# Kernel tuning notes

Hardware: AMD Instinct MI355X
Metric: run time of the kernel (lower is better)

## Reference

```python
import jax, jax.numpy as jnp
import numpy as np

N_HEADS = 8
N_HIDDEN = 64  # out_features // n_heads
SLOPE = 0.2
NEG = -9e15


def setup_inputs() -> dict:
    key = jax.random.key(0)
    k1, k2, k3, k4, k5 = jax.random.split(key, 5)
    B, N, F_in, F_out = 4, 2048, 512, 512
    h = jax.random.normal(k1, (B, N, F_in), dtype=jnp.float32)
    adj = jax.random.randint(k2, (B, N, N), 0, 2, dtype=jnp.int32)
    # xavier_uniform with gain=1.414: limit = gain*sqrt(6/(fan_in+fan_out))
    lim_W = 1.414 * np.sqrt(6.0 / (F_in + F_out))
    W_l = jax.random.uniform(k3, (F_in, F_out), jnp.float32, -lim_W, lim_W)
    W_r = jax.random.uniform(k4, (F_in, F_out), jnp.float32, -lim_W, lim_W)
    lim_a = 1.414 * np.sqrt(6.0 / (N_HIDDEN + 1))
    a = jax.random.uniform(k5, (N_HIDDEN, 1), jnp.float32, -lim_a, lim_a)
    return {"h": h, "adj": adj, "W_l": W_l, "W_r": W_r, "a": a}


def reference(h, adj, W_l, W_r, a):
    B, N, _ = h.shape
    H, d = N_HEADS, N_HIDDEN
    # torch .view(-1, H, N, d) is a raw row-major reshape, replicated exactly here
    Wh_l = jax.nn.leaky_relu((h @ W_l).reshape(B, H, N, d), SLOPE)
    Wh_r = jax.nn.leaky_relu((h @ W_r).reshape(B, H, N, d), SLOPE)
    # e: [B,H,N,1] + [B,H,1,N] -> [B,H,N,N]
    e = Wh_l @ a + jnp.swapaxes(Wh_r @ a, 2, 3)
    att = jnp.where(adj[:, None, :, :] > 0, e, NEG)
    att = jax.nn.softmax(att, axis=-1)
    h_prime = att @ Wh_r  # [B,H,N,d]
    # torch .view(-1, N, H*d): raw reshape (no head transpose)
    out = jax.nn.elu(h_prime.reshape(B, N, H * d))
    return out
```

## Files before the change

kernel.cpp:

```cpp
#include <hip/hip_runtime.h>

#define NB   4
#define NN   2048
#define FIN  512
#define FOUT 512
#define NHD  8
#define DH   64
#define VC   576
#define SLOPE 0.2f

typedef __attribute__((ext_vector_type(8)))  short bhalf8;
typedef __attribute__((ext_vector_type(16))) float f32x16;

__device__ __forceinline__ void load_lds16(const void* g, void* l) {
  __builtin_amdgcn_global_load_lds(
      (const __attribute__((address_space(1))) unsigned int*)g,
      (__attribute__((address_space(3))) unsigned int*)l, 16, 0, 0);
}

__device__ __forceinline__ unsigned int bfpair(float lo, float hi) {
  unsigned int a = __float_as_uint(lo), b = __float_as_uint(hi);
  a = (a + 0x7FFFu + ((a >> 16) & 1u)) >> 16;
  b = (b + 0x7FFFu + ((b >> 16) & 1u)) & 0xFFFF0000u;
  return a | b;
}

__device__ __forceinline__ void split2(float x, float y,
                                       unsigned int& hp, unsigned int& lp) {
  unsigned int ux = __float_as_uint(x), uy = __float_as_uint(y);
  unsigned int rx = (ux + 0x7FFFu + ((ux >> 16) & 1u)) & 0xFFFF0000u;
  unsigned int ry = (uy + 0x7FFFu + ((uy >> 16) & 1u)) & 0xFFFF0000u;
  float lx = x - __uint_as_float(rx);
  float ly = y - __uint_as_float(ry);
  unsigned int vx = __float_as_uint(lx), vy = __float_as_uint(ly);
  hp = (rx >> 16) | ry;
  lp = ((vx + 0x7FFFu + ((vx >> 16) & 1u)) >> 16)
     | ((vy + 0x7FFFu + ((vy >> 16) & 1u)) & 0xFFFF0000u);
}

__global__ __launch_bounds__(256) void k_split_prep(
    const float* __restrict__ h,
    unsigned short* __restrict__ hHi, unsigned short* __restrict__ hLo,
    const float* __restrict__ Wr,
    unsigned short* __restrict__ wTh, unsigned short* __restrict__ wTl)
{
  __shared__ float s[64][65];
  const int t = threadIdx.x;
  if (blockIdx.x < 2048) {
    size_t base = ((size_t)blockIdx.x * 256 + t) * 8;
    float4 a = *(const float4*)(h + base);
    float4 b = *(const float4*)(h + base + 4);
    uint4 uh, ul;
    split2(a.x, a.y, uh.x, ul.x);
    split2(a.z, a.w, uh.y, ul.y);
    split2(b.x, b.y, uh.z, ul.z);
    split2(b.z, b.w, uh.w, ul.w);
    *(uint4*)(hHi + base) = uh;
    *(uint4*)(hLo + base) = ul;
    return;
  }
  const int bid2 = blockIdx.x - 2048;
  const int n0 = (bid2 & 7) * 64, k0 = (bid2 >> 3) * 64;
#pragma unroll
  for (int p = 0; p < 4; ++p) {
    int row = p * 16 + (t >> 4);
    int col = (t & 15) * 4;
    float4 v = *(const float4*)(Wr + (size_t)(k0 + row) * FOUT + n0 + col);
    s[row][col] = v.x; s[row][col+1] = v.y; s[row][col+2] = v.z; s[row][col+3] = v.w;
  }
  __syncthreads();
  const int n = t >> 2;
  const int ks = (t & 3) * 16;
  uint4 h0, h1, l0, l1;
  split2(s[ks+ 0][n], s[ks+ 1][n], h0.x, l0.x);
  split2(s[ks+ 2][n], s[ks+ 3][n], h0.y, l0.y);
  split2(s[ks+ 4][n], s[ks+ 5][n], h0.z, l0.z);
  split2(s[ks+ 6][n], s[ks+ 7][n], h0.w, l0.w);
  split2(s[ks+ 8][n], s[ks+ 9][n], h1.x, l1.x);
  split2(s[ks+10][n], s[ks+11][n], h1.y, l1.y);
  split2(s[ks+12][n], s[ks+13][n], h1.z, l1.z);
  split2(s[ks+14][n], s[ks+15][n], h1.w, l1.w);
  size_t o = (size_t)(n0 + n) * FIN + k0 + ks;
  *(uint4*)(wTh + o) = h0; *(uint4*)(wTh + o + 8) = h1;
  *(uint4*)(wTl + o) = l0; *(uint4*)(wTl + o + 8) = l1;
}

__global__ __launch_bounds__(256) void k_gemm_whr_mfma(
    const unsigned short* __restrict__ hHi, const unsigned short* __restrict__ hLo,
    const unsigned short* __restrict__ wTh, const unsigned short* __restrict__ wTl,
    float* __restrict__ Whr, const float* __restrict__ av, float* __restrict__ er)
{
  __shared__ unsigned short sAh[128*64], sAl[128*64];
  __shared__ unsigned short sBh[64*64],  sBl[64*64];
  const int tid = threadIdx.x, lane = tid & 63, wv = tid >> 6;
  const int Bid = blockIdx.x;
  const int g8 = Bid & 7, idx = Bid >> 3;
  const int sg = idx >> 3, ct = idx & 7;
  const int c0 = ct * 64;
  const int row0 = (g8 * 8 + sg) * 128;

  const unsigned short* pAh[4]; const unsigned short* pAl[4];
  unsigned short *dAh[4], *dAl[4];
#pragma unroll
  for (int t = 0; t < 4; ++t) {
    int I  = wv + t * 4;
    int rl = I * 8 + (lane >> 3);
    int gk = (lane & 7) ^ (rl & 7);
    pAh[t] = hHi + (size_t)(row0 + rl) * FIN + gk * 8;
    pAl[t] = hLo + (size_t)(row0 + rl) * FIN + gk * 8;
    dAh[t] = sAh + I * 512;  dAl[t] = sAl + I * 512;
  }
  const unsigned short* pBh[2]; const unsigned short* pBl[2];
  unsigned short *dBh[2], *dBl[2];
#pragma unroll
  for (int t = 0; t < 2; ++t) {
    int I  = wv + t * 4;
    int rl = I * 8 + (lane >> 3);
    int gk = (lane & 7) ^ (rl & 7);
    pBh[t] = wTh + (size_t)(c0 + rl) * FIN + gk * 8;
    pBl[t] = wTl + (size_t)(c0 + rl) * FIN + gk * 8;
    dBh[t] = sBh + I * 512;  dBl[t] = sBl + I * 512;
  }

  const int wi = wv >> 1, wc = wv & 1;
  const int l31 = lane & 31, half = lane >> 5;
  const int aoff0 = (wi*64 +      l31) * 64;
  const int aoff1 = (wi*64 + 32 + l31) * 64;
  const int boff  = (wc*32 +      l31) * 64;
  f32x16 acc0 = {}; f32x16 acc1 = {};

  for (int k0 = 0; k0 < FIN; k0 += 64) {
#pragma unroll
    for (int t = 0; t < 4; ++t) { load_lds16(pAh[t] + k0, dAh[t]);
                                  load_lds16(pAl[t] + k0, dAl[t]); }
#pragma unroll
    for (int t = 0; t < 2; ++t) { load_lds16(pBh[t] + k0, dBh[t]);
                                  load_lds16(pBl[t] + k0, dBl[t]); }
    __syncthreads();
#pragma unroll
    for (int kb = 0; kb < 4; ++kb) {
      int kg = ((kb*2 + half) ^ (lane & 7)) * 8;
      bhalf8 bh  = *(const bhalf8*)&sBh[boff  + kg];
      bhalf8 bl  = *(const bhalf8*)&sBl[boff  + kg];
      bhalf8 a0h = *(const bhalf8*)&sAh[aoff0 + kg];
      bhalf8 a0l = *(const bhalf8*)&sAl[aoff0 + kg];
      bhalf8 a1h = *(const bhalf8*)&sAh[aoff1 + kg];
      bhalf8 a1l = *(const bhalf8*)&sAl[aoff1 + kg];
      acc0 = __builtin_amdgcn_mfma_f32_32x32x16_bf16(a0h, bh, acc0, 0, 0, 0);
      acc1 = __builtin_amdgcn_mfma_f32_32x32x16_bf16(a1h, bh, acc1, 0, 0, 0);
      acc0 = __builtin_amdgcn_mfma_f32_32x32x16_bf16(a0l, bh, acc0, 0, 0, 0);
      acc1 = __builtin_amdgcn_mfma_f32_32x32x16_bf16(a1l, bh, acc1, 0, 0, 0);
      acc0 = __builtin_amdgcn_mfma_f32_32x32x16_bf16(a0h, bl, acc0, 0, 0, 0);
      acc1 = __builtin_amdgcn_mfma_f32_32x32x16_bf16(a1h, bl, acc1, 0, 0, 0);
    }
    __syncthreads();
  }

  const float a_d = av[wc*32 + l31];
#pragma unroll
  for (int mi = 0; mi < 2; ++mi) {
    const f32x16 a = mi ? acc1 : acc0;
#pragma unroll
    for (int reg = 0; reg < 16; ++reg) {
      int grow = row0 + wi*64 + mi*32 + ((reg & 3) + 8*(reg >> 2) + 4*half);
      int b  = grow >> 11;
      int n  = grow & 2047;
      int hd = n >> 8;
      int jj = ((n & 255) << 3) | ct;
      int dd = wc*32 + l31;
      float v = a[reg];
      v = v > 0.f ? v : SLOPE * v;
      Whr[(((size_t)(b*NHD + hd)) * NN + jj) * DH + dd] = v;
      float p = v * a_d;
      p += __shfl_xor(p, 16, 32);
      p += __shfl_xor(p,  8, 32);
      p += __shfl_xor(p,  4, 32);
      p += __shfl_xor(p,  2, 32);
      p += __shfl_xor(p,  1, 32);
      if (l31 == 0)
        unsafeAtomicAdd(er + ((size_t)(b*NHD + hd)) * NN + jj, p);
    }
  }
}

__global__ __launch_bounds__(256) void k_softmax_w(float* __restrict__ er)
{
  __shared__ float wm[4];
  float* p = er + (size_t)blockIdx.x * NN;
  float m = -1e30f;
  for (int j = threadIdx.x; j < NN; j += 256) m = fmaxf(m, p[j]);
#pragma unroll
  for (int off = 32; off; off >>= 1) m = fmaxf(m, __shfl_down(m, off, 64));
  if ((threadIdx.x & 63) == 0) wm[threadIdx.x >> 6] = m;
  __syncthreads();
  float mm = fmaxf(fmaxf(wm[0], wm[1]), fmaxf(wm[2], wm[3]));
  for (int j = threadIdx.x; j < NN; j += 256) p[j] = expf(p[j] - mm);
}

__global__ __launch_bounds__(256) void k_build_vt(
    const float* __restrict__ Whr, const float* __restrict__ w,
    unsigned short* __restrict__ Vt)
{
  const int lane = threadIdx.x & 63, wv = threadIdx.x >> 6;
  const int c = blockIdx.y * 4 + wv;
  const int b = blockIdx.z;
  const int j = blockIdx.x * 512 + lane * 8;
  uint4 o = {0u, 0u, 0u, 0u};
  if (c < 512) {
    const int hh = c >> 6, dd = c & 63;
    const size_t r = ((size_t)(b*NHD + hh))*NN + j;
    const float* wp = w + r;
    const float* hp = Whr + r*DH + dd;
    float v[8];
#pragma unroll
    for (int q = 0; q < 8; ++q) v[q] = wp[q] * hp[(size_t)q*DH];
    o.x = bfpair(v[0], v[1]); o.y = bfpair(v[2], v[3]);
    o.z = bfpair(v[4], v[5]); o.w = bfpair(v[6], v[7]);
  } else if (c < 520) {
    const size_t r = ((size_t)(b*NHD + (c - 512)))*NN + j;
    float4 a0 = *(const float4*)(w + r);
    float4 a1 = *(const float4*)(w + r + 4);
    o.x = bfpair(a0.x, a0.y); o.y = bfpair(a0.z, a0.w);
    o.z = bfpair(a1.x, a1.y); o.w = bfpair(a1.z, a1.w);
  }
  *(uint4*)(Vt + ((size_t)(b*VC + c))*NN + j) = o;
}

__global__ __launch_bounds__(256) void k_attn_mfma(
    const int* __restrict__ adj, const unsigned short* __restrict__ Vt,
    float* __restrict__ C)
{
  __shared__ unsigned short sA[128][72];
  __shared__ unsigned short sB[64][64];
  const int tid = threadIdx.x;
  const int lane = tid & 63, wv = tid >> 6;
  const int Bid = blockIdx.x;
  const int g8 = Bid & 7;
  const int kh = (Bid >> 3) & 1;
  const int idx = Bid >> 4;
  const int ct = idx >> 3, sg = idx & 7;
  const int c0 = ct * 64;
  const int row0 = (g8 * 8 + sg) * 128;
  const int b = row0 >> 11;

  const unsigned short* pB[2];
  unsigned short* dB[2];
#pragma unroll
  for (int t = 0; t < 2; ++t) {
    int I  = wv + t*4;
    int rl = I*8 + (lane >> 3);
    int gk = (lane & 7) ^ (rl & 7);
    pB[t] = Vt + ((size_t)(b*VC + c0 + rl))*NN + gk*8;
    dB[t] = &sB[0][0] + I*512;
  }
  const int* adjp = adj + (size_t)b*NN*NN + (size_t)(row0 & 2047)*NN
                    + (tid >> 3)*NN + (tid & 7)*8;
  unsigned short* sAp = &sA[tid >> 3][(tid & 7)*8];

  const int wi = wv >> 1, wc = wv & 1;
  const int l31 = lane & 31, half = lane >> 5;
  f32x16 acc0 = {}; f32x16 acc1 = {};
  const unsigned short* aRd0 = &sA[wi*64 +      l31][half*8];
  const unsigned short* aRd1 = &sA[wi*64 + 32 + l31][half*8];
  const int nloc = wc*32 + l31;

  const int kbeg = kh * 1024, kend = kbeg + 1024;
  for (int k0 = kbeg; k0 < kend; k0 += 64) {
    load_lds16(pB[0] + k0, dB[0]);
    load_lds16(pB[1] + k0, dB[1]);
#pragma unroll
    for (int rr = 0; rr < 4; ++rr) {
      const int* p = adjp + rr*32*NN + k0;
      int4 q0 = *(const int4*)p;
      int4 q1 = *(const int4*)(p + 4);
      uint4 u;
      u.x = (unsigned)(q0.x | (q0.y << 16)) * 0x3F80u;
      u.y = (unsigned)(q0.z | (q0.w << 16)) * 0x3F80u;
      u.z = (unsigned)(q1.x | (q1.y << 16)) * 0x3F80u;
      u.w = (unsigned)(q1.z | (q1.w << 16)) * 0x3F80u;
      *(uint4*)(sAp + rr*32*72) = u;
    }
    __syncthreads();
#pragma unroll
    for (int kb = 0; kb < 4; ++kb) {
      int kg = (kb*2 + half) ^ (lane & 7);
      bhalf8 bf = *(const bhalf8*)&sB[nloc][kg*8];
      bhalf8 a0 = *(const bhalf8*)(aRd0 + kb*16);
      bhalf8 a1 = *(const bhalf8*)(aRd1 + kb*16);
      acc0 = __builtin_amdgcn_mfma_f32_32x32x16_bf16(a0, bf, acc0, 0, 0, 0);
      acc1 = __builtin_amdgcn_mfma_f32_32x32x16_bf16(a1, bf, acc1, 0, 0, 0);
    }
    __syncthreads();
  }
  float* Cp = C + ((size_t)(row0 + wi*64))*VC + c0 + wc*32 + l31;
#pragma unroll
  for (int mi = 0; mi < 2; ++mi) {
    const f32x16 a = mi ? acc1 : acc0;
#pragma unroll
    for (int reg = 0; reg < 16; ++reg) {
      int irow = (reg & 3) + 8*(reg >> 2) + 4*half + mi*32;
      unsafeAtomicAdd(Cp + (size_t)irow * VC, a[reg]);
    }
  }
}

__global__ __launch_bounds__(256) void k_epilogue(
    const float* __restrict__ C, float* __restrict__ out)
{
  int idx = blockIdx.x * 256 + threadIdx.x;
  int d  = idx & 63;
  int t  = idx >> 6;
  int hh = t & 7;
  int bi = t >> 3;
  int i  = bi & 2047, b = bi >> 11;
  float num = C[(size_t)bi * VC + (hh << 6) + d];
  float den = C[(size_t)bi * VC + 512 + hh];
  float v = num / den;
  v = v > 0.f ? v : expm1f(v);
  int n = (hh << 8) | (i >> 3);
  int f = ((i & 7) << 6) | d;
  out[((size_t)b * NN + n) * FOUT + f] = v;
}

extern "C" void kernel_launch(void* const* d_in, const int* in_sizes, int n_in,
                              void* d_out, int out_size, void* d_ws, size_t ws_size,
                              hipStream_t stream)
{
  const float* hin = (const float*)d_in[0];
  const int*   adj = (const int*)d_in[1];
  const float* Wr  = (const float*)d_in[3];
  const float* av  = (const float*)d_in[4];
  float* out = (float*)d_out;

  char* ws = (char*)d_ws;
  unsigned short* hHi = (unsigned short*)(ws);
  unsigned short* hLo = (unsigned short*)(ws + 8388608);
  unsigned short* wTh = (unsigned short*)(ws + 16777216);
  unsigned short* wTl = (unsigned short*)(ws + 17301504);
  float* Whr  = (float*)(ws + 17825792);
  float* wexp = (float*)(ws + 34603008);
  unsigned short* Vt = (unsigned short*)(ws);
  float* C    = (float*)(ws + 17825792);

  hipMemsetAsync(wexp, 0, (size_t)NB*NHD*NN*4, stream);
  k_split_prep   <<<dim3(2112),           256, 0, stream>>>(hin, hHi, hLo, Wr, wTh, wTl);
  k_gemm_whr_mfma<<<dim3(512),            256, 0, stream>>>(hHi, hLo, wTh, wTl, Whr, av, wexp);
  k_softmax_w    <<<dim3(NB*NHD),         256, 0, stream>>>(wexp);
  k_build_vt     <<<dim3(NN/512, VC/4, NB), 256, 0, stream>>>(Whr, wexp, Vt);
  hipMemsetAsync(C, 0, (size_t)NB*NN*VC*4, stream);
  k_attn_mfma    <<<dim3(1152),           256, 0, stream>>>(adj, Vt, C);
  k_epilogue     <<<dim3(NB*NN*FOUT/256), 256, 0, stream>>>(C, out);
}
```

Measured before the change: 237.8 us.

## Fuse softmax weights, Vt build and epilogue into attention pipeline, drop atomics

The softmax-exponent and Vt-build kernels are merged into one kernel that transposes through shared memory to write coalesced bf16 Vt rows. The attention kernel no longer splits K across two blocks. It computes the denominator with an extra MFMA per K-step and applies the divide and ELU directly, removing the C buffer, both memsets, the atomic accumulation and the separate epilogue kernel. The GEMM's er reduction now goes through LDS with a plain store instead of atomics. The tradeoffs are half as many attention blocks (512 vs 1152), each doing a full-length K loop, and every softmax block recomputing the per-row max.

New measurement: 198.8 us. 1.2x faster.

```diff
diff --git a/kernel.cpp b/kernel.cpp
--- a/kernel.cpp
+++ b/kernel.cpp
@@ -6,7 +6,7 @@
 #define FOUT 512
 #define NHD  8
 #define DH   64
-#define VC   576
+#define VTR  520
 #define SLOPE 0.2f
 
 typedef __attribute__((ext_vector_type(8)))  short bhalf8;
@@ -18,11 +18,9 @@
       (__attribute__((address_space(3))) unsigned int*)l, 16, 0, 0);
 }
 
-__device__ __forceinline__ unsigned int bfpair(float lo, float hi) {
-  unsigned int a = __float_as_uint(lo), b = __float_as_uint(hi);
-  a = (a + 0x7FFFu + ((a >> 16) & 1u)) >> 16;
-  b = (b + 0x7FFFu + ((b >> 16) & 1u)) & 0xFFFF0000u;
-  return a | b;
+__device__ __forceinline__ unsigned short bfrne(float x) {
+  unsigned int u = __float_as_uint(x);
+  return (unsigned short)((u + 0x7FFFu + ((u >> 16) & 1u)) >> 16);
 }
 
 __device__ __forceinline__ void split2(float x, float y,
@@ -92,6 +90,7 @@
 {
   __shared__ unsigned short sAh[128*64], sAl[128*64];
   __shared__ unsigned short sBh[64*64],  sBl[64*64];
+  __shared__ float erT[128][2];
   const int tid = threadIdx.x, lane = tid & 63, wv = tid >> 6;
   const int Bid = blockIdx.x;
   const int g8 = Bid & 7, idx = Bid >> 3;
@@ -162,112 +161,130 @@
     const f32x16 a = mi ? acc1 : acc0;
 #pragma unroll
     for (int reg = 0; reg < 16; ++reg) {
-      int grow = row0 + wi*64 + mi*32 + ((reg & 3) + 8*(reg >> 2) + 4*half);
+      int rmap = (reg & 3) + 8*(reg >> 2) + 4*half;
+      int rowloc = wi*64 + mi*32 + rmap;
+      int grow = row0 + rowloc;
       int b  = grow >> 11;
       int n  = grow & 2047;
       int hd = n >> 8;
       int jj = ((n & 255) << 3) | ct;
-      int dd = wc*32 + l31;
       float v = a[reg];
       v = v > 0.f ? v : SLOPE * v;
-      Whr[(((size_t)(b*NHD + hd)) * NN + jj) * DH + dd] = v;
+      Whr[(((size_t)(b*NHD + hd)) * NN + jj) * DH + (wc*32 + l31)] = v;
       float p = v * a_d;
       p += __shfl_xor(p, 16, 32);
       p += __shfl_xor(p,  8, 32);
       p += __shfl_xor(p,  4, 32);
       p += __shfl_xor(p,  2, 32);
       p += __shfl_xor(p,  1, 32);
-      if (l31 == 0)
-        unsafeAtomicAdd(er + ((size_t)(b*NHD + hd)) * NN + jj, p);
-    }
-  }
-}
-
-__global__ __launch_bounds__(256) void k_softmax_w(float* __restrict__ er)
+      if (l31 == 0) erT[rowloc][wc] = p;
+    }
+  }
+  __syncthreads();
+  if (tid < 128) {
+    int grow = row0 + tid;
+    int b  = grow >> 11;
+    int n  = grow & 2047;
+    int hd = n >> 8;
+    int jj = ((n & 255) << 3) | ct;
+    er[((size_t)(b*NHD + hd)) * NN + jj] = erT[tid][0] + erT[tid][1];
+  }
+}
+
+__global__ __launch_bounds__(256) void k_softvt(
+    const float* __restrict__ Whr, const float* __restrict__ er,
+    unsigned short* __restrict__ Vt)
 {
   __shared__ float wm[4];
-  float* p = er + (size_t)blockIdx.x * NN;
+  __shared__ float wbuf[256];
+  __shared__ unsigned short tile[64][264];
+  const int tid = threadIdx.x;
+  const int jc = blockIdx.x, hh = blockIdx.y, b = blockIdx.z;
+  const float* ep = er + ((size_t)(b*NHD + hh)) * NN;
   float m = -1e30f;
-  for (int j = threadIdx.x; j < NN; j += 256) m = fmaxf(m, p[j]);
+  for (int j = tid; j < NN; j += 256) m = fmaxf(m, ep[j]);
 #pragma unroll
   for (int off = 32; off; off >>= 1) m = fmaxf(m, __shfl_down(m, off, 64));
-  if ((threadIdx.x & 63) == 0) wm[threadIdx.x >> 6] = m;
-  __syncthreads();
-  float mm = fmaxf(fmaxf(wm[0], wm[1]), fmaxf(wm[2], wm[3]));
-  for (int j = threadIdx.x; j < NN; j += 256) p[j] = expf(p[j] - mm);
-}
-
-__global__ __launch_bounds__(256) void k_build_vt(
-    const float* __restrict__ Whr, const float* __restrict__ w,
-    unsigned short* __restrict__ Vt)
-{
-  const int lane = threadIdx.x & 63, wv = threadIdx.x >> 6;
-  const int c = blockIdx.y * 4 + wv;
-  const int b = blockIdx.z;
-  const int j = blockIdx.x * 512 + lane * 8;
-  uint4 o = {0u, 0u, 0u, 0u};
-  if (c < 512) {
-    const int hh = c >> 6, dd = c & 63;
-    const size_t r = ((size_t)(b*NHD + hh))*NN + j;
-    const float* wp = w + r;
-    const float* hp = Whr + r*DH + dd;
-    float v[8];
-#pragma unroll
-    for (int q = 0; q < 8; ++q) v[q] = wp[q] * hp[(size_t)q*DH];
-    o.x = bfpair(v[0], v[1]); o.y = bfpair(v[2], v[3]);
-    o.z = bfpair(v[4], v[5]); o.w = bfpair(v[6], v[7]);
-  } else if (c < 520) {
-    const size_t r = ((size_t)(b*NHD + (c - 512)))*NN + j;
-    float4 a0 = *(const float4*)(w + r);
-    float4 a1 = *(const float4*)(w + r + 4);
-    o.x = bfpair(a0.x, a0.y); o.y = bfpair(a0.z, a0.w);
-    o.z = bfpair(a1.x, a1.y); o.w = bfpair(a1.z, a1.w);
-  }
-  *(uint4*)(Vt + ((size_t)(b*VC + c))*NN + j) = o;
-}
-
-__global__ __launch_bounds__(256) void k_attn_mfma(
+  if ((tid & 63) == 0) wm[tid >> 6] = m;
+  __syncthreads();
+  const float mm = fmaxf(fmaxf(wm[0], wm[1]), fmaxf(wm[2], wm[3]));
+  const int j0 = jc * 256;
+  float w = expf(ep[j0 + tid] - mm);
+  wbuf[tid] = w;
+  Vt[((size_t)(b*VTR + 512 + hh)) * NN + j0 + tid] = bfrne(w);
+  __syncthreads();
+  const size_t wbase = ((size_t)(b*NHD + hh)) * NN;
+#pragma unroll
+  for (int p = 0; p < 16; ++p) {
+    int jr = p*16 + (tid >> 4);
+    int dc = (tid & 15) * 4;
+    float4 v = *(const float4*)(Whr + (wbase + j0 + jr) * DH + dc);
+    float wj = wbuf[jr];
+    tile[dc+0][jr] = bfrne(v.x * wj);
+    tile[dc+1][jr] = bfrne(v.y * wj);
+    tile[dc+2][jr] = bfrne(v.z * wj);
+    tile[dc+3][jr] = bfrne(v.w * wj);
+  }
+  __syncthreads();
+#pragma unroll
+  for (int q = 0; q < 8; ++q) {
+    int idx = q*256 + tid;
+    int d = idx >> 5, seg = idx & 31;
+    uint4 t16 = *(const uint4*)&tile[d][seg*8];
+    *(uint4*)(Vt + ((size_t)(b*VTR + hh*64 + d)) * NN + j0 + seg*8) = t16;
+  }
+}
+
+__global__ __launch_bounds__(256) void k_attn_out(
     const int* __restrict__ adj, const unsigned short* __restrict__ Vt,
-    float* __restrict__ C)
+    float* __restrict__ out)
 {
   __shared__ unsigned short sA[128][72];
-  __shared__ unsigned short sB[64][64];
+  __shared__ unsigned short sB[96][64];
+  __shared__ float denL[128];
   const int tid = threadIdx.x;
   const int lane = tid & 63, wv = tid >> 6;
   const int Bid = blockIdx.x;
-  const int g8 = Bid & 7;
-  const int kh = (Bid >> 3) & 1;
-  const int idx = Bid >> 4;
-  const int ct = idx >> 3, sg = idx & 7;
-  const int c0 = ct * 64;
-  const int row0 = (g8 * 8 + sg) * 128;
+  const int g8 = Bid & 7, rest = Bid >> 3;
+  const int ct = rest & 7, sg = rest >> 3;
+  const int row0 = (g8*8 + sg) * 128;
   const int b = row0 >> 11;
 
-  const unsigned short* pB[2];
-  unsigned short* dB[2];
+  const unsigned short* pB[3];
+  unsigned short* dB[3];
 #pragma unroll
   for (int t = 0; t < 2; ++t) {
     int I  = wv + t*4;
     int rl = I*8 + (lane >> 3);
     int gk = (lane & 7) ^ (rl & 7);
-    pB[t] = Vt + ((size_t)(b*VC + c0 + rl))*NN + gk*8;
+    pB[t] = Vt + ((size_t)(b*VTR + ct*64 + rl))*NN + gk*8;
     dB[t] = &sB[0][0] + I*512;
   }
+  {
+    int x  = lane >> 3;
+    int gk = (lane & 7) ^ (x & 7);
+    pB[2] = Vt + ((size_t)(b*VTR + 512 + x))*NN + gk*8;
+    dB[2] = &sB[0][0] + 8*512;
+  }
+  for (int idx = tid; idx < 384; idx += 256)
+    ((uint4*)&sB[72][0])[idx] = uint4{0u,0u,0u,0u};
+
   const int* adjp = adj + (size_t)b*NN*NN + (size_t)(row0 & 2047)*NN
                     + (tid >> 3)*NN + (tid & 7)*8;
   unsigned short* sAp = &sA[tid >> 3][(tid & 7)*8];
 
   const int wi = wv >> 1, wc = wv & 1;
   const int l31 = lane & 31, half = lane >> 5;
-  f32x16 acc0 = {}; f32x16 acc1 = {};
+  f32x16 acc0 = {}; f32x16 acc1 = {}; f32x16 acc2 = {};
   const unsigned short* aRd0 = &sA[wi*64 +      l31][half*8];
   const unsigned short* aRd1 = &sA[wi*64 + 32 + l31][half*8];
+  const unsigned short* aRd2 = &sA[wv*32 +      l31][half*8];
   const int nloc = wc*32 + l31;
 
-  const int kbeg = kh * 1024, kend = kbeg + 1024;
-  for (int k0 = kbeg; k0 < kend; k0 += 64) {
+  for (int k0 = 0; k0 < NN; k0 += 64) {
     load_lds16(pB[0] + k0, dB[0]);
     load_lds16(pB[1] + k0, dB[1]);
+    if (wv == 0) load_lds16(pB[2] + k0, dB[2]);
 #pragma unroll
     for (int rr = 0; rr < 4; ++rr) {
       const int* p = adjp + rr*32*NN + k0;
@@ -284,42 +301,38 @@
 #pragma unroll
     for (int kb = 0; kb < 4; ++kb) {
       int kg = (kb*2 + half) ^ (lane & 7);
-      bhalf8 bf = *(const bhalf8*)&sB[nloc][kg*8];
+      bhalf8 bf  = *(const bhalf8*)&sB[nloc][kg*8];
+      bhalf8 bf2 = *(const bhalf8*)&sB[64 + l31][kg*8];
       bhalf8 a0 = *(const bhalf8*)(aRd0 + kb*16);
       bhalf8 a1 = *(const bhalf8*)(aRd1 + kb*16);
-      acc0 = __builtin_amdgcn_mfma_f32_32x32x16_bf16(a0, bf, acc0, 0, 0, 0);
-      acc1 = __builtin_amdgcn_mfma_f32_32x32x16_bf16(a1, bf, acc1, 0, 0, 0);
+      bhalf8 a2 = *(const bhalf8*)(aRd2 + kb*16);
+      acc0 = __builtin_amdgcn_mfma_f32_32x32x16_bf16(a0, bf,  acc0, 0, 0, 0);
+      acc1 = __builtin_amdgcn_mfma_f32_32x32x16_bf16(a1, bf,  acc1, 0, 0, 0);
+      acc2 = __builtin_amdgcn_mfma_f32_32x32x16_bf16(a2, bf2, acc2, 0, 0, 0);
     }
     __syncthreads();
   }
-  float* Cp = C + ((size_t)(row0 + wi*64))*VC + c0 + wc*32 + l31;
+  if (l31 == ct) {
+#pragma unroll
+    for (int reg = 0; reg < 16; ++reg)
+      denL[wv*32 + (reg & 3) + 8*(reg >> 2) + 4*half] = acc2[reg];
+  }
+  __syncthreads();
+  const int ib = row0 & 2047;
 #pragma unroll
   for (int mi = 0; mi < 2; ++mi) {
     const f32x16 a = mi ? acc1 : acc0;
 #pragma unroll
     for (int reg = 0; reg < 16; ++reg) {
-      int irow = (reg & 3) + 8*(reg >> 2) + 4*half + mi*32;
-      unsafeAtomicAdd(Cp + (size_t)irow * VC, a[reg]);
-    }
-  }
-}
-
-__global__ __launch_bounds__(256) void k_epilogue(
-    const float* __restrict__ C, float* __restrict__ out)
-{
-  int idx = blockIdx.x * 256 + threadIdx.x;
-  int d  = idx & 63;
-  int t  = idx >> 6;
-  int hh = t & 7;
-  int bi = t >> 3;
-  int i  = bi & 2047, b = bi >> 11;
-  float num = C[(size_t)bi * VC + (hh << 6) + d];
-  float den = C[(size_t)bi * VC + 512 + hh];
-  float v = num / den;
-  v = v > 0.f ? v : expm1f(v);
-  int n = (hh << 8) | (i >> 3);
-  int f = ((i & 7) << 6) | d;
-  out[((size_t)b * NN + n) * FOUT + f] = v;
+      int il = wi*64 + mi*32 + (reg & 3) + 8*(reg >> 2) + 4*half;
+      int i  = ib + il;
+      float v = a[reg] / denL[il];
+      v = v > 0.f ? v : expm1f(v);
+      int n = (ct << 8) | (i >> 3);
+      int f = ((i & 7) << 6) | nloc;
+      out[((size_t)b*NN + n)*FOUT + f] = v;
+    }
+  }
 }
 
 extern "C" void kernel_launch(void* const* d_in, const int* in_sizes, int n_in,
@@ -338,16 +351,11 @@
   unsigned short* wTh = (unsigned short*)(ws + 16777216);
   unsigned short* wTl = (unsigned short*)(ws + 17301504);
   float* Whr  = (float*)(ws + 17825792);
-  float* wexp = (float*)(ws + 34603008);
+  float* er   = (float*)(ws + 34603008);
   unsigned short* Vt = (unsigned short*)(ws);
-  float* C    = (float*)(ws + 17825792);
-
-  hipMemsetAsync(wexp, 0, (size_t)NB*NHD*NN*4, stream);
-  k_split_prep   <<<dim3(2112),           256, 0, stream>>>(hin, hHi, hLo, Wr, wTh, wTl);
-  k_gemm_whr_mfma<<<dim3(512),            256, 0, stream>>>(hHi, hLo, wTh, wTl, Whr, av, wexp);
-  k_softmax_w    <<<dim3(NB*NHD),         256, 0, stream>>>(wexp);
-  k_build_vt     <<<dim3(NN/512, VC/4, NB), 256, 0, stream>>>(Whr, wexp, Vt);
-  hipMemsetAsync(C, 0, (size_t)NB*NN*VC*4, stream);
-  k_attn_mfma    <<<dim3(1152),           256, 0, stream>>>(adj, Vt, C);
-  k_epilogue     <<<dim3(NB*NN*FOUT/256), 256, 0, stream>>>(C, out);
-}
+
+  k_split_prep   <<<dim3(2112),    256, 0, stream>>>(hin, hHi, hLo, Wr, wTh, wTl);
+  k_gemm_whr_mfma<<<dim3(512),     256, 0, stream>>>(hHi, hLo, wTh, wTl, Whr, av, er);
+  k_softvt       <<<dim3(8, 8, 4), 256, 0, stream>>>(Whr, er, Vt);
+  k_attn_out     <<<dim3(512),     256, 0, stream>>>(adj, Vt, out);
+}
```
